# Performance work log

Measured on AMD Instinct MI355X. Metric: run time of the kernel, lower is better.

Reference implementation:

```python
import jax, jax.numpy as jnp
import numpy as np
from functools import partial

H = 50  # hidden size hardcoded in the module


def _lstm_cell(x, h, c, W_ih, W_hh, b_ih, b_hh):
    # PyTorch LSTMCell math, gate order i, f, g, o
    gates = x @ W_ih.T + h @ W_hh.T + b_ih + b_hh  # [B, 4H]
    i, f, g, o = jnp.split(gates, 4, axis=-1)
    c_new = jax.nn.sigmoid(f) * c + jax.nn.sigmoid(i) * jnp.tanh(g)
    h_new = jax.nn.sigmoid(o) * jnp.tanh(c_new)
    return h_new, c_new


def setup_inputs() -> dict:
    key = jax.random.key(0)
    ks = jax.random.split(key, 11)
    B, T = 512, 1024

    def w(k, shape, fan_in):
        return (jax.random.normal(k, shape, jnp.float32) / np.sqrt(fan_in)).astype(jnp.float32)

    return {
        "x": jax.random.normal(ks[0], (B, T), jnp.float32),
        "W_ih1": w(ks[1], (4 * H, 1), H),
        "W_hh1": w(ks[2], (4 * H, H), H),
        "b_ih1": w(ks[3], (4 * H,), H),
        "b_hh1": w(ks[4], (4 * H,), H),
        "W_ih2": w(ks[5], (4 * H, H), H),
        "W_hh2": w(ks[6], (4 * H, H), H),
        "b_ih2": w(ks[7], (4 * H,), H),
        "b_hh2": w(ks[8], (4 * H,), H),
        "W_lin": w(ks[9], (1, H), H),
        "b_lin": w(ks[10], (1,), H),
        "predict": 32,
    }


def reference(x, W_ih1, W_hh1, b_ih1, b_hh1, W_ih2, W_hh2, b_ih2, b_hh2,
              W_lin, b_lin, predict):
    B = x.shape[0]
    z = jnp.zeros((B, H), x.dtype)
    init = (z, z, z, z)

    def step(carry, x_t):  # x_t: [B, 1]
        h1, c1, h2, c2 = carry
        h1, c1 = _lstm_cell(x_t, h1, c1, W_ih1, W_hh1, b_ih1, b_hh1)
        h2, c2 = _lstm_cell(h1, h2, c2, W_ih2, W_hh2, b_ih2, b_hh2)
        out = h2 @ W_lin.T + b_lin  # [B, 1]
        return (h1, c1, h2, c2), out

    xs = jnp.swapaxes(x, 0, 1)[:, :, None]  # [T, B, 1]
    carry, outs = jax.lax.scan(step, init, xs)  # outs: [T, B, 1]

    if predict > 0:
        h1, c1, h2, c2 = carry

        def pstep(pcarry, _):
            h1, c1, h2, c2, o = pcarry
            h1, c1 = _lstm_cell(o, h1, c1, W_ih1, W_hh1, b_ih1, b_hh1)
            h2, c2 = _lstm_cell(h1, h2, c2, W_ih2, W_hh2, b_ih2, b_hh2)
            out = h2 @ W_lin.T + b_lin
            return (h1, c1, h2, c2, out), out

        _, pouts = jax.lax.scan(pstep, (h1, c1, h2, c2, outs[-1]), None, length=predict)
        outs = jnp.concatenate([outs, pouts], axis=0)

    # stack(dim=1).squeeze(2) -> [B, T + predict]
    return jnp.swapaxes(outs[..., 0], 0, 1)
```

## Files before the change

kernel.cpp:

```cpp
#include <hip/hip_runtime.h>


#define Hh   50
#define TLEN 1024

typedef _Float16 half2v __attribute__((ext_vector_type(2)));

#if __has_builtin(__builtin_amdgcn_fdot2)
#define FDOT2(a, b, c) __builtin_amdgcn_fdot2((a), (b), (c), false)
#else
#define FDOT2(a, b, c) ((c) + (float)(a)[0] * (float)(b)[0] + (float)(a)[1] * (float)(b)[1])
#endif

#define BC(f) __builtin_bit_cast(half2v, f)

__device__ __forceinline__ float fast_sigmoid(float v) {
    return 1.0f / (1.0f + __expf(-v));
}
__device__ __forceinline__ float fast_tanh(float v) {
    return 1.0f - 2.0f / (__expf(2.0f * v) + 1.0f);
}

extern "C" __global__ __launch_bounds__(128, 1)
void sine_lstm_kernel(const float* __restrict__ x,
                      const float* __restrict__ W_ih1,
                      const float* __restrict__ W_hh1,
                      const float* __restrict__ b_ih1,
                      const float* __restrict__ b_hh1,
                      const float* __restrict__ W_ih2,
                      const float* __restrict__ W_hh2,
                      const float* __restrict__ b_ih2,
                      const float* __restrict__ b_hh2,
                      const float* __restrict__ W_lin,
                      const float* __restrict__ b_lin,
                      const int*   __restrict__ predict_p,
                      float* __restrict__ out,
                      int T)
{
    __shared__ __align__(16) float    x_lds[TLEN];
    __shared__ __align__(16) _Float16 h1lds[2][64];
    __shared__ __align__(16) _Float16 h2lds[2][64];
    __shared__ __align__(16) float    h2f32[2][64];

    const int tid = threadIdx.x;
    const int wv  = tid >> 6;
    const int ln  = tid & 63;
    const bool isProd = (wv == 0);
    const int b   = blockIdx.x;
    const int predict = *predict_p;
    const int S = T + predict;

    for (int i = tid; i < TLEN; i += 128)
        x_lds[i] = x[(size_t)b * T + i];
    ((_Float16*)h1lds)[tid] = (_Float16)0.0f;
    ((_Float16*)h2lds)[tid] = (_Float16)0.0f;
    ((float*)h2f32)[tid] = 0.0f;

    const bool act = (ln < Hh);

    const float* MA = isProd ? W_hh1 : W_ih2;
    const float* MB = isProd ? W_hh1 : W_hh2;
    half2v wgtA[4][25], wgtB[4][25];
    float  bv[4], wih[4];
    #pragma unroll
    for (int q = 0; q < 4; ++q) {
        const int r = act ? (q * Hh + ln) : 0;
        bv[q]  = isProd ? (b_ih1[r] + b_hh1[r]) : (b_ih2[r] + b_hh2[r]);
        wih[q] = W_ih1[r];
        #pragma unroll
        for (int p = 0; p < 25; ++p) {
            wgtA[q][p] = half2v{(_Float16)MA[r * Hh + 2*p], (_Float16)MA[r * Hh + 2*p + 1]};
            wgtB[q][p] = half2v{(_Float16)MB[r * Hh + 2*p], (_Float16)MB[r * Hh + 2*p + 1]};
        }
    }
    const float wlin_l = act ? W_lin[ln] : 0.0f;
    const float blin   = b_lin[0];
    float cst = 0.0f;

    __syncthreads();

    for (int t = 0; t <= S; ++t) {
        __syncthreads();
        const bool pred = (t >= T);

        if (!isProd && t >= 1) {
            float acc[4][4];
            #pragma unroll
            for (int q = 0; q < 4; ++q) {
                acc[q][0] = bv[q]; acc[q][1] = 0.0f; acc[q][2] = 0.0f; acc[q][3] = 0.0f;
            }
            const int s1 = (t + 1) & 1;
            #pragma unroll
            for (int L = 0; L < 6; ++L) {
                float4 f = *(const float4*)&h1lds[s1][8 * L];
                #pragma unroll
                for (int j = 0; j < 4; ++j) {
                    const float hj = (&f.x)[j];
                    #pragma unroll
                    for (int q = 0; q < 4; ++q)
                        acc[q][j] = FDOT2(wgtA[q][4*L + j], BC(hj), acc[q][j]);
                }
            }
            {
                const float h24 = *(const float*)&h1lds[s1][48];
                #pragma unroll
                for (int q = 0; q < 4; ++q)
                    acc[q][0] = FDOT2(wgtA[q][24], BC(h24), acc[q][0]);
            }
            const int s2 = t & 1;
            #pragma unroll
            for (int L = 0; L < 6; ++L) {
                float4 f = *(const float4*)&h2lds[s2][8 * L];
                #pragma unroll
                for (int j = 0; j < 4; ++j) {
                    const float hj = (&f.x)[j];
                    #pragma unroll
                    for (int q = 0; q < 4; ++q)
                        acc[q][j] = FDOT2(wgtB[q][4*L + j], BC(hj), acc[q][j]);
                }
            }
            {
                const float h24 = *(const float*)&h2lds[s2][48];
                #pragma unroll
                for (int q = 0; q < 4; ++q)
                    acc[q][0] = FDOT2(wgtB[q][24], BC(h24), acc[q][0]);
            }
            float gi = (acc[0][0] + acc[0][2]) + (acc[0][1] + acc[0][3]);
            float gf = (acc[1][0] + acc[1][2]) + (acc[1][1] + acc[1][3]);
            float gg = (acc[2][0] + acc[2][2]) + (acc[2][1] + acc[2][3]);
            float go = (acc[3][0] + acc[3][2]) + (acc[3][1] + acc[3][3]);
            if (act) {
                float cn = fast_sigmoid(gf) * cst + fast_sigmoid(gi) * fast_tanh(gg);
                cst = cn;
                float hn = fast_sigmoid(go) * fast_tanh(cn);
                h2lds[(t + 1) & 1][ln] = (_Float16)hn;
                h2f32[(t + 1) & 1][ln] = hn;
            }
        }

        if (isProd && t >= 2 && t <= T) {
            float part = act ? h2f32[t & 1][ln] * wlin_l : 0.0f;
            #pragma unroll
            for (int off = 32; off > 0; off >>= 1)
                part += __shfl_down(part, off);
            if (ln == 0) out[(size_t)b * S + (t - 2)] = part + blin;
        }

        if (!pred) {
            if (isProd) {
                const float xin = x_lds[t];
                float acc[4][4];
                #pragma unroll
                for (int q = 0; q < 4; ++q) {
                    acc[q][0] = bv[q] + xin * wih[q];
                    acc[q][1] = 0.0f; acc[q][2] = 0.0f; acc[q][3] = 0.0f;
                }
                const int s1 = (t + 1) & 1;
                #pragma unroll
                for (int L = 0; L < 6; ++L) {
                    float4 f = *(const float4*)&h1lds[s1][8 * L];
                    #pragma unroll
                    for (int j = 0; j < 4; ++j) {
                        const float hj = (&f.x)[j];
                        #pragma unroll
                        for (int q = 0; q < 4; ++q)
                            acc[q][j] = FDOT2(wgtA[q][4*L + j], BC(hj), acc[q][j]);
                    }
                }
                {
                    const float h24 = *(const float*)&h1lds[s1][48];
                    #pragma unroll
                    for (int q = 0; q < 4; ++q)
                        acc[q][0] = FDOT2(wgtA[q][24], BC(h24), acc[q][0]);
                }
                float gi = (acc[0][0] + acc[0][2]) + (acc[0][1] + acc[0][3]);
                float gf = (acc[1][0] + acc[1][2]) + (acc[1][1] + acc[1][3]);
                float gg = (acc[2][0] + acc[2][2]) + (acc[2][1] + acc[2][3]);
                float go = (acc[3][0] + acc[3][2]) + (acc[3][1] + acc[3][3]);
                if (act) {
                    float cn = fast_sigmoid(gf) * cst + fast_sigmoid(gi) * fast_tanh(gg);
                    cst = cn;
                    h1lds[t & 1][ln] = (_Float16)(fast_sigmoid(go) * fast_tanh(cn));
                }
            }
        } else {
            __syncthreads();
            float part = act ? h2f32[(t + 1) & 1][ln] * wlin_l : 0.0f;
            #pragma unroll
            for (int off = 32; off > 0; off >>= 1)
                part += __shfl_down(part, off);
            float o = __shfl(part, 0) + blin;
            if (tid == 0) out[(size_t)b * S + (t - 1)] = o;
            if (isProd && t < S) {
                float acc[4][4];
                #pragma unroll
                for (int q = 0; q < 4; ++q) {
                    acc[q][0] = bv[q] + o * wih[q];
                    acc[q][1] = 0.0f; acc[q][2] = 0.0f; acc[q][3] = 0.0f;
                }
                const int s1 = (t + 1) & 1;
                #pragma unroll
                for (int L = 0; L < 6; ++L) {
                    float4 f = *(const float4*)&h1lds[s1][8 * L];
                    #pragma unroll
                    for (int j = 0; j < 4; ++j) {
                        const float hj = (&f.x)[j];
                        #pragma unroll
                        for (int q = 0; q < 4; ++q)
                            acc[q][j] = FDOT2(wgtA[q][4*L + j], BC(hj), acc[q][j]);
                    }
                }
                {
                    const float h24 = *(const float*)&h1lds[s1][48];
                    #pragma unroll
                    for (int q = 0; q < 4; ++q)
                        acc[q][0] = FDOT2(wgtA[q][24], BC(h24), acc[q][0]);
                }
                float gi = (acc[0][0] + acc[0][2]) + (acc[0][1] + acc[0][3]);
                float gf = (acc[1][0] + acc[1][2]) + (acc[1][1] + acc[1][3]);
                float gg = (acc[2][0] + acc[2][2]) + (acc[2][1] + acc[2][3]);
                float go = (acc[3][0] + acc[3][2]) + (acc[3][1] + acc[3][3]);
                if (act) {
                    float cn = fast_sigmoid(gf) * cst + fast_sigmoid(gi) * fast_tanh(gg);
                    cst = cn;
                    h1lds[t & 1][ln] = (_Float16)(fast_sigmoid(go) * fast_tanh(cn));
                }
            }
        }
    }
}

extern "C" void kernel_launch(void* const* d_in, const int* in_sizes, int n_in,
                              void* d_out, int out_size, void* d_ws, size_t ws_size,
                              hipStream_t stream) {
    const float* x      = (const float*)d_in[0];
    const float* W_ih1  = (const float*)d_in[1];
    const float* W_hh1  = (const float*)d_in[2];
    const float* b_ih1  = (const float*)d_in[3];
    const float* b_hh1  = (const float*)d_in[4];
    const float* W_ih2  = (const float*)d_in[5];
    const float* W_hh2  = (const float*)d_in[6];
    const float* b_ih2  = (const float*)d_in[7];
    const float* b_hh2  = (const float*)d_in[8];
    const float* W_lin  = (const float*)d_in[9];
    const float* b_lin  = (const float*)d_in[10];
    const int*   pred   = (const int*)d_in[11];
    float* out = (float*)d_out;

    const int B = 512;
    const int T = in_sizes[0] / B;

    dim3 grid(B), block(128);
    hipLaunchKernelGGL(sine_lstm_kernel, grid, block, 0, stream,
                       x, W_ih1, W_hh1, b_ih1, b_hh1,
                       W_ih2, W_hh2, b_ih2, b_hh2,
                       W_lin, b_lin, pred, out, T);
}
```

Before: 930.6 us.

## Rebalance layer-2 input matvec between waves and shadow hidden state in registers

The producer wave now computes half of layer 2's W_ih2·h1 product (the first 24 columns) right after producing h1, and passes those partial gate sums to the consumer wave through a double-buffered LDS array. The consumer then only does the remaining 26 columns plus W_hh2·h2. This balances per-step FDOT2 work between the two waves, which were previously uneven (50 vs 100 columns). Each wave also keeps a register copy of its own recurrent hidden state, refilled from LDS right after it writes, so the recurrent matvec reads registers instead of issuing LDS loads. The cost is an extra 16-float LDS store and load per lane per step, plus more register pressure.

```diff
diff --git a/kernel.cpp b/kernel.cpp
--- a/kernel.cpp
+++ b/kernel.cpp
@@ -20,6 +20,20 @@
 __device__ __forceinline__ float fast_tanh(float v) {
     return 1.0f - 2.0f / (__expf(2.0f * v) + 1.0f);
 }
+__device__ __forceinline__ void lds_fence() {
+    asm volatile("" ::: "memory");
+    __builtin_amdgcn_sched_barrier(0);
+}
+
+#define SHADOW(CARRY, BUF, SLOT) do {                                        \
+    _Pragma("unroll")                                                        \
+    for (int L_ = 0; L_ < 6; ++L_) {                                         \
+        float4 f_ = *(const float4*)&BUF[SLOT][8 * L_];                      \
+        CARRY[4*L_] = f_.x; CARRY[4*L_+1] = f_.y;                            \
+        CARRY[4*L_+2] = f_.z; CARRY[4*L_+3] = f_.w;                          \
+    }                                                                        \
+    CARRY[24] = *(const float*)&BUF[SLOT][48];                               \
+} while (0)
 
 extern "C" __global__ __launch_bounds__(128, 1)
 void sine_lstm_kernel(const float* __restrict__ x,
@@ -41,6 +55,7 @@
     __shared__ __align__(16) _Float16 h1lds[2][64];
     __shared__ __align__(16) _Float16 h2lds[2][64];
     __shared__ __align__(16) float    h2f32[2][64];
+    __shared__ __align__(16) float    part[2][4][64][4];
 
     const int tid = threadIdx.x;
     const int wv  = tid >> 6;
@@ -58,23 +73,31 @@
 
     const bool act = (ln < Hh);
 
-    const float* MA = isProd ? W_hh1 : W_ih2;
-    const float* MB = isProd ? W_hh1 : W_hh2;
-    half2v wgtA[4][25], wgtB[4][25];
-    float  bv[4], wih[4];
+    const float* MA = isProd ? W_hh1 : W_hh2;
+    const int    pbase = isProd ? 0 : 12;
+    half2v wgtA[4][25], wgtB[4][13];
+    float  b1v[4], b2v[4], wih[4];
     #pragma unroll
     for (int q = 0; q < 4; ++q) {
         const int r = act ? (q * Hh + ln) : 0;
-        bv[q]  = isProd ? (b_ih1[r] + b_hh1[r]) : (b_ih2[r] + b_hh2[r]);
+        b1v[q] = b_ih1[r] + b_hh1[r];
+        b2v[q] = b_ih2[r] + b_hh2[r];
         wih[q] = W_ih1[r];
         #pragma unroll
-        for (int p = 0; p < 25; ++p) {
+        for (int p = 0; p < 25; ++p)
             wgtA[q][p] = half2v{(_Float16)MA[r * Hh + 2*p], (_Float16)MA[r * Hh + 2*p + 1]};
-            wgtB[q][p] = half2v{(_Float16)MB[r * Hh + 2*p], (_Float16)MB[r * Hh + 2*p + 1]};
+        #pragma unroll
+        for (int p = 0; p < 13; ++p) {
+            const int k0 = 2 * (pbase + p);
+            wgtB[q][p] = half2v{(_Float16)W_ih2[r * Hh + k0], (_Float16)W_ih2[r * Hh + k0 + 1]};
         }
     }
     const float wlin_l = act ? W_lin[ln] : 0.0f;
     const float blin   = b_lin[0];
+
+    float hc[25];
+    #pragma unroll
+    for (int p = 0; p < 25; ++p) hc[p] = 0.0f;
     float cst = 0.0f;
 
     __syncthreads();
@@ -84,47 +107,43 @@
         const bool pred = (t >= T);
 
         if (!isProd && t >= 1) {
+            const int sp = (t + 1) & 1;
             float acc[4][4];
             #pragma unroll
             for (int q = 0; q < 4; ++q) {
-                acc[q][0] = bv[q]; acc[q][1] = 0.0f; acc[q][2] = 0.0f; acc[q][3] = 0.0f;
-            }
-            const int s1 = (t + 1) & 1;
+                float4 pr = *(const float4*)&part[sp][q][ln][0];
+                acc[q][0] = pr.x; acc[q][1] = pr.y; acc[q][2] = pr.z; acc[q][3] = pr.w;
+            }
+            #pragma unroll
+            for (int L = 3; L < 6; ++L) {
+                float4 f = *(const float4*)&h1lds[sp][8 * L];
+                #pragma unroll
+                for (int j = 0; j < 4; ++j) {
+                    const float hj = (&f.x)[j];
+                    #pragma unroll
+                    for (int q = 0; q < 4; ++q)
+                        acc[q][j] = FDOT2(wgtB[q][4*(L-3) + j], BC(hj), acc[q][j]);
+                }
+            }
+            {
+                const float h24 = *(const float*)&h1lds[sp][48];
+                #pragma unroll
+                for (int q = 0; q < 4; ++q)
+                    acc[q][0] = FDOT2(wgtB[q][12], BC(h24), acc[q][0]);
+            }
             #pragma unroll
             for (int L = 0; L < 6; ++L) {
-                float4 f = *(const float4*)&h1lds[s1][8 * L];
-                #pragma unroll
-                for (int j = 0; j < 4; ++j) {
-                    const float hj = (&f.x)[j];
+                #pragma unroll
+                for (int j = 0; j < 4; ++j) {
+                    const float hj = hc[4*L + j];
                     #pragma unroll
                     for (int q = 0; q < 4; ++q)
                         acc[q][j] = FDOT2(wgtA[q][4*L + j], BC(hj), acc[q][j]);
                 }
             }
-            {
-                const float h24 = *(const float*)&h1lds[s1][48];
-                #pragma unroll
-                for (int q = 0; q < 4; ++q)
-                    acc[q][0] = FDOT2(wgtA[q][24], BC(h24), acc[q][0]);
-            }
-            const int s2 = t & 1;
-            #pragma unroll
-            for (int L = 0; L < 6; ++L) {
-                float4 f = *(const float4*)&h2lds[s2][8 * L];
-                #pragma unroll
-                for (int j = 0; j < 4; ++j) {
-                    const float hj = (&f.x)[j];
-                    #pragma unroll
-                    for (int q = 0; q < 4; ++q)
-                        acc[q][j] = FDOT2(wgtB[q][4*L + j], BC(hj), acc[q][j]);
-                }
-            }
-            {
-                const float h24 = *(const float*)&h2lds[s2][48];
-                #pragma unroll
-                for (int q = 0; q < 4; ++q)
-                    acc[q][0] = FDOT2(wgtB[q][24], BC(h24), acc[q][0]);
-            }
+            #pragma unroll
+            for (int q = 0; q < 4; ++q)
+                acc[q][0] = FDOT2(wgtA[q][24], BC(hc[24]), acc[q][0]);
             float gi = (acc[0][0] + acc[0][2]) + (acc[0][1] + acc[0][3]);
             float gf = (acc[1][0] + acc[1][2]) + (acc[1][1] + acc[1][3]);
             float gg = (acc[2][0] + acc[2][2]) + (acc[2][1] + acc[2][3]);
@@ -136,96 +155,83 @@
                 h2lds[(t + 1) & 1][ln] = (_Float16)hn;
                 h2f32[(t + 1) & 1][ln] = hn;
             }
+            lds_fence();
+            SHADOW(hc, h2lds, (t + 1) & 1);
         }
 
         if (isProd && t >= 2 && t <= T) {
-            float part = act ? h2f32[t & 1][ln] * wlin_l : 0.0f;
+            float pt = act ? h2f32[t & 1][ln] * wlin_l : 0.0f;
             #pragma unroll
             for (int off = 32; off > 0; off >>= 1)
-                part += __shfl_down(part, off);
-            if (ln == 0) out[(size_t)b * S + (t - 2)] = part + blin;
-        }
-
+                pt += __shfl_down(pt, off);
+            if (ln == 0) out[(size_t)b * S + (t - 2)] = pt + blin;
+        }
+
+        float xin = 0.0f;
+        bool doG1 = false;
         if (!pred) {
-            if (isProd) {
-                const float xin = x_lds[t];
-                float acc[4][4];
-                #pragma unroll
-                for (int q = 0; q < 4; ++q) {
-                    acc[q][0] = bv[q] + xin * wih[q];
-                    acc[q][1] = 0.0f; acc[q][2] = 0.0f; acc[q][3] = 0.0f;
-                }
-                const int s1 = (t + 1) & 1;
-                #pragma unroll
-                for (int L = 0; L < 6; ++L) {
-                    float4 f = *(const float4*)&h1lds[s1][8 * L];
-                    #pragma unroll
-                    for (int j = 0; j < 4; ++j) {
-                        const float hj = (&f.x)[j];
-                        #pragma unroll
-                        for (int q = 0; q < 4; ++q)
-                            acc[q][j] = FDOT2(wgtA[q][4*L + j], BC(hj), acc[q][j]);
-                    }
-                }
-                {
-                    const float h24 = *(const float*)&h1lds[s1][48];
-                    #pragma unroll
-                    for (int q = 0; q < 4; ++q)
-                        acc[q][0] = FDOT2(wgtA[q][24], BC(h24), acc[q][0]);
-                }
-                float gi = (acc[0][0] + acc[0][2]) + (acc[0][1] + acc[0][3]);
-                float gf = (acc[1][0] + acc[1][2]) + (acc[1][1] + acc[1][3]);
-                float gg = (acc[2][0] + acc[2][2]) + (acc[2][1] + acc[2][3]);
-                float go = (acc[3][0] + acc[3][2]) + (acc[3][1] + acc[3][3]);
-                if (act) {
-                    float cn = fast_sigmoid(gf) * cst + fast_sigmoid(gi) * fast_tanh(gg);
-                    cst = cn;
-                    h1lds[t & 1][ln] = (_Float16)(fast_sigmoid(go) * fast_tanh(cn));
-                }
-            }
+            if (isProd) { xin = x_lds[t]; doG1 = true; }
         } else {
             __syncthreads();
-            float part = act ? h2f32[(t + 1) & 1][ln] * wlin_l : 0.0f;
+            float pt = act ? h2f32[(t + 1) & 1][ln] * wlin_l : 0.0f;
             #pragma unroll
             for (int off = 32; off > 0; off >>= 1)
-                part += __shfl_down(part, off);
-            float o = __shfl(part, 0) + blin;
+                pt += __shfl_down(pt, off);
+            float o = __shfl(pt, 0) + blin;
             if (tid == 0) out[(size_t)b * S + (t - 1)] = o;
-            if (isProd && t < S) {
-                float acc[4][4];
-                #pragma unroll
-                for (int q = 0; q < 4; ++q) {
-                    acc[q][0] = bv[q] + o * wih[q];
-                    acc[q][1] = 0.0f; acc[q][2] = 0.0f; acc[q][3] = 0.0f;
-                }
-                const int s1 = (t + 1) & 1;
-                #pragma unroll
-                for (int L = 0; L < 6; ++L) {
-                    float4 f = *(const float4*)&h1lds[s1][8 * L];
-                    #pragma unroll
-                    for (int j = 0; j < 4; ++j) {
-                        const float hj = (&f.x)[j];
-                        #pragma unroll
-                        for (int q = 0; q < 4; ++q)
-                            acc[q][j] = FDOT2(wgtA[q][4*L + j], BC(hj), acc[q][j]);
-                    }
-                }
-                {
-                    const float h24 = *(const float*)&h1lds[s1][48];
-                    #pragma unroll
-                    for (int q = 0; q < 4; ++q)
-                        acc[q][0] = FDOT2(wgtA[q][24], BC(h24), acc[q][0]);
-                }
-                float gi = (acc[0][0] + acc[0][2]) + (acc[0][1] + acc[0][3]);
-                float gf = (acc[1][0] + acc[1][2]) + (acc[1][1] + acc[1][3]);
-                float gg = (acc[2][0] + acc[2][2]) + (acc[2][1] + acc[2][3]);
-                float go = (acc[3][0] + acc[3][2]) + (acc[3][1] + acc[3][3]);
-                if (act) {
-                    float cn = fast_sigmoid(gf) * cst + fast_sigmoid(gi) * fast_tanh(gg);
-                    cst = cn;
-                    h1lds[t & 1][ln] = (_Float16)(fast_sigmoid(go) * fast_tanh(cn));
-                }
-            }
+            if (isProd && t < S) { xin = o; doG1 = true; }
+        }
+
+        if (doG1) {
+            float acc[4][4];
+            #pragma unroll
+            for (int q = 0; q < 4; ++q) {
+                acc[q][0] = b1v[q] + xin * wih[q];
+                acc[q][1] = 0.0f; acc[q][2] = 0.0f; acc[q][3] = 0.0f;
+            }
+            #pragma unroll
+            for (int L = 0; L < 6; ++L) {
+                #pragma unroll
+                for (int j = 0; j < 4; ++j) {
+                    const float hj = hc[4*L + j];
+                    #pragma unroll
+                    for (int q = 0; q < 4; ++q)
+                        acc[q][j] = FDOT2(wgtA[q][4*L + j], BC(hj), acc[q][j]);
+                }
+            }
+            #pragma unroll
+            for (int q = 0; q < 4; ++q)
+                acc[q][0] = FDOT2(wgtA[q][24], BC(hc[24]), acc[q][0]);
+            float gi = (acc[0][0] + acc[0][2]) + (acc[0][1] + acc[0][3]);
+            float gf = (acc[1][0] + acc[1][2]) + (acc[1][1] + acc[1][3]);
+            float gg = (acc[2][0] + acc[2][2]) + (acc[2][1] + acc[2][3]);
+            float go = (acc[3][0] + acc[3][2]) + (acc[3][1] + acc[3][3]);
+            if (act) {
+                float cn = fast_sigmoid(gf) * cst + fast_sigmoid(gi) * fast_tanh(gg);
+                cst = cn;
+                h1lds[t & 1][ln] = (_Float16)(fast_sigmoid(go) * fast_tanh(cn));
+            }
+            lds_fence();
+            SHADOW(hc, h1lds, t & 1);
+            float pa[4][4];
+            #pragma unroll
+            for (int q = 0; q < 4; ++q) {
+                pa[q][0] = b2v[q]; pa[q][1] = 0.0f; pa[q][2] = 0.0f; pa[q][3] = 0.0f;
+            }
+            #pragma unroll
+            for (int L = 0; L < 3; ++L) {
+                #pragma unroll
+                for (int j = 0; j < 4; ++j) {
+                    const float hj = hc[4*L + j];
+                    #pragma unroll
+                    for (int q = 0; q < 4; ++q)
+                        pa[q][j] = FDOT2(wgtB[q][4*L + j], BC(hj), pa[q][j]);
+                }
+            }
+            #pragma unroll
+            for (int q = 0; q < 4; ++q)
+                *(float4*)&part[t & 1][q][ln][0] =
+                    make_float4(pa[q][0], pa[q][1], pa[q][2], pa[q][3]);
         }
     }
 }
```

After: 1.148 ms. 1.23x slower.
